# Performance work log

Measured on AMD Instinct MI355X. Metric: run time of the kernel, lower is better.

## Reference

```python
import jax, jax.numpy as jnp
import numpy as np

# Fixed-step Dormand-Prince RK45 (dopri5) over t in [0, 1].
# torchdiffeq's dopri5 is adaptive; an adaptive while-loop is not
# reverse-differentiable in JAX, so we use the same dopri5 tableau with a
# fixed step count, which reproduces the per-step math exactly.
N_STEPS = 64

# dopri5 Butcher tableau (a-matrix rows; b = 5th-order weights = row a7)
A21 = 1/5
A31, A32 = 3/40, 9/40
A41, A42, A43 = 44/45, -56/15, 32/9
A51, A52, A53, A54 = 19372/6561, -25360/2187, 64448/6561, -212/729
A61, A62, A63, A64, A65 = 9017/3168, -355/33, 46732/5247, 49/176, -5103/18656
B1, B3, B4, B5, B6 = 35/384, 500/1113, 125/192, -2187/6784, 11/84


def setup_inputs() -> dict:
    key = jax.random.key(0)
    ks = jax.random.split(key, 7)
    data_dim, hidden_dim, batch = 512, 1024, 4096
    s1 = 1.0 / np.sqrt(data_dim)
    s2 = 1.0 / np.sqrt(hidden_dim)
    return {
        "x":  jax.random.normal(ks[0], (batch, data_dim), jnp.float32),
        "W1": jax.random.normal(ks[1], (hidden_dim, data_dim), jnp.float32) * s1,
        "b1": jax.random.normal(ks[2], (hidden_dim,), jnp.float32) * s1,
        "W2": jax.random.normal(ks[3], (hidden_dim, hidden_dim), jnp.float32) * s2,
        "b2": jax.random.normal(ks[4], (hidden_dim,), jnp.float32) * s2,
        "W3": jax.random.normal(ks[5], (data_dim, hidden_dim), jnp.float32) * s2,
        "b3": jax.random.normal(ks[6], (data_dim,), jnp.float32) * s2,
    }


def reference(x, W1, b1, W2, b2, W3, b3):
    def f(y):  # ODEFunc MLP: fc1 -> relu -> fc2 -> relu -> fc3 (autonomous)
        h = jax.nn.relu(y @ W1.T + b1)
        h = jax.nn.relu(h @ W2.T + b2)
        return h @ W3.T + b3

    h = jnp.float32(1.0 / N_STEPS)

    def step(y, _):
        k1 = f(y)
        k2 = f(y + h * (A21 * k1))
        k3 = f(y + h * (A31 * k1 + A32 * k2))
        k4 = f(y + h * (A41 * k1 + A42 * k2 + A43 * k3))
        k5 = f(y + h * (A51 * k1 + A52 * k2 + A53 * k3 + A54 * k4))
        k6 = f(y + h * (A61 * k1 + A62 * k2 + A63 * k3 + A64 * k4 + A65 * k5))
        y_next = y + h * (B1 * k1 + B3 * k3 + B4 * k4 + B5 * k5 + B6 * k6)
        return y_next, None

    y_final, _ = jax.lax.scan(step, x, None, length=N_STEPS)
    return y_final
```

## Files before the change

### kernel.cpp

```cpp
#include <hip/hip_runtime.h>
#include <hip/hip_bf16.h>
#include <stdint.h>
#include <stddef.h>

using bf16_t = __hip_bfloat16;
typedef __attribute__((ext_vector_type(8))) short short8;
typedef __attribute__((ext_vector_type(4))) float f32x4;

__device__ __forceinline__ void gload_lds16(void* lds, const void* g) {
  __builtin_amdgcn_global_load_lds(
      (const __attribute__((address_space(1))) unsigned int*)g,
      (__attribute__((address_space(3))) unsigned int*)lds,
      16, 0, 0);
}

template<bool RELU, bool COMBINE, bool STORE_K, bool STORE_YF>
__global__ __launch_bounds__(256, 4)
void gemm_bt(const bf16_t* __restrict__ A, const bf16_t* __restrict__ B,
             const float* __restrict__ bias,
             bf16_t* __restrict__ obf,
             bf16_t* __restrict__ kout,
             float* __restrict__ yf_out,
             const float* __restrict__ y_in,
             const bf16_t* __restrict__ kp0, const bf16_t* __restrict__ kp1,
             const bf16_t* __restrict__ kp2, const bf16_t* __restrict__ kp3,
             float c0, float c1, float c2, float c3, float ccur,
             int M, int N, int K, int lgx)
{
  __shared__ __align__(16) bf16_t As[2][64 * 64];
  __shared__ __align__(16) bf16_t Bs[2][64 * 64];

  const int t    = threadIdx.x;
  const int lane = t & 63;
  const int wid  = t >> 6;
  const int wm   = wid >> 1;
  const int wn   = wid & 1;

  const int nwg = gridDim.x, bid = blockIdx.x;
  const int swz = (bid & 7) * (nwg >> 3) + (bid >> 3);
  const int gxm = (1 << lgx) - 1;
  const int bx  = swz & gxm;
  const int by  = swz >> lgx;
  const int bn0 = bx * 64, bm0 = by * 64;

  const bf16_t* Ag = A + (size_t)bm0 * K;
  const bf16_t* Bg = B + (size_t)bn0 * K;

  f32x4 acc[2][2] = {};

  auto stage = [&](int b, int kt) {
    const int k0 = kt * 64;
#pragma unroll
    for (int r = 0; r < 2; ++r) {
      int ch  = t + r * 256;
      int row = ch >> 3, s = ch & 7;
      int sl  = s ^ (row & 7);
      gload_lds16(&As[b][ch * 8], Ag + (size_t)row * K + k0 + sl * 8);
    }
#pragma unroll
    for (int r = 0; r < 2; ++r) {
      int ch  = t + r * 256;
      int row = ch >> 3, s = ch & 7;
      int sl  = s ^ (row & 7);
      gload_lds16(&Bs[b][ch * 8], Bg + (size_t)row * K + k0 + sl * 8);
    }
  };

  const int nt = K >> 6;
  stage(0, 0);

  const int ro = lane & 15;
  const int ks = lane >> 4;

  for (int tt = 0; tt < nt; ++tt) {
    const int c = tt & 1;
    asm volatile("s_waitcnt vmcnt(0)" ::: "memory");
    __builtin_amdgcn_s_barrier();
    asm volatile("" ::: "memory");

    if (tt + 1 < nt) stage(c ^ 1, tt + 1);

#pragma unroll
    for (int kk = 0; kk < 2; ++kk) {
      short8 af[2], bfr[2];
      const int slot = kk * 4 + ks;
#pragma unroll
      for (int mi = 0; mi < 2; ++mi) {
        int row = wm * 32 + mi * 16 + ro;
        int ch  = row * 8 + (slot ^ (row & 7));
        af[mi]  = *(const short8*)&As[c][ch * 8];
      }
#pragma unroll
      for (int ni = 0; ni < 2; ++ni) {
        int row = wn * 32 + ni * 16 + ro;
        int ch  = row * 8 + (slot ^ (row & 7));
        bfr[ni] = *(const short8*)&Bs[c][ch * 8];
      }
      __builtin_amdgcn_s_setprio(1);
#pragma unroll
      for (int mi = 0; mi < 2; ++mi)
#pragma unroll
        for (int ni = 0; ni < 2; ++ni)
          acc[mi][ni] = __builtin_amdgcn_mfma_f32_16x16x32_bf16(
              af[mi], bfr[ni], acc[mi][ni], 0, 0, 0);
      __builtin_amdgcn_s_setprio(0);
    }
  }

  const int rb = bm0 + wm * 32;
  const int cb = bn0 + wn * 32;
#pragma unroll
  for (int mi = 0; mi < 2; ++mi) {
#pragma unroll
    for (int ni = 0; ni < 2; ++ni) {
      const int col = cb + ni * 16 + ro;
      const float bv = bias[col];
#pragma unroll
      for (int r = 0; r < 4; ++r) {
        const int row = rb + mi * 16 + (lane >> 4) * 4 + r;
        const size_t idx = (size_t)row * N + col;
        float v = acc[mi][ni][r] + bv;
        if (RELU) v = fmaxf(v, 0.f);
        if (COMBINE) {
          if (STORE_K) kout[idx] = __float2bfloat16(v);
          float z = y_in[idx] + ccur * v;
          if (kp0) z += c0 * __bfloat162float(kp0[idx]);
          if (kp1) z += c1 * __bfloat162float(kp1[idx]);
          if (kp2) z += c2 * __bfloat162float(kp2[idx]);
          if (kp3) z += c3 * __bfloat162float(kp3[idx]);
          if (STORE_YF) yf_out[idx] = z;
          obf[idx] = __float2bfloat16(z);
        } else {
          obf[idx] = __float2bfloat16(v);
        }
      }
    }
  }
}

__global__ void init_y_kernel(const float* __restrict__ x, float* __restrict__ y,
                              bf16_t* __restrict__ yb, int n) {
  int i = blockIdx.x * blockDim.x + threadIdx.x;
  if (i < n) {
    float v = x[i];
    y[i]  = v;
    yb[i] = __float2bfloat16(v);
  }
}

__global__ void f2b_kernel(const float* __restrict__ in, bf16_t* __restrict__ out, int n) {
  int i = blockIdx.x * blockDim.x + threadIdx.x;
  if (i < n) out[i] = __float2bfloat16(in[i]);
}

extern "C" void kernel_launch(void* const* d_in, const int* in_sizes, int n_in,
                              void* d_out, int out_size, void* d_ws, size_t ws_size,
                              hipStream_t stream)
{
  const float* x  = (const float*)d_in[0];
  const float* W1 = (const float*)d_in[1];
  const float* b1 = (const float*)d_in[2];
  const float* W2 = (const float*)d_in[3];
  const float* b2 = (const float*)d_in[4];
  const float* W3 = (const float*)d_in[5];
  const float* b3 = (const float*)d_in[6];

  const int data   = in_sizes[6];
  const int hidden = in_sizes[2];
  const int batch  = in_sizes[0] / data;

  char* ws = (char*)d_ws;
  size_t off = 0;
  auto alloc = [&](size_t bytes) -> void* {
    off = (off + 255) & ~(size_t)255;
    void* p = ws + off;
    off += bytes;
    return p;
  };
  const size_t nyd = (size_t)batch * data;
  const size_t nh  = (size_t)batch * hidden;

  float*  y   = (float*)alloc(nyd * 4);
  bf16_t* yb  = (bf16_t*)alloc(nyd * 2);
  bf16_t* zb  = (bf16_t*)alloc(nyd * 2);
  bf16_t* h1  = (bf16_t*)alloc(nh * 2);
  bf16_t* h2  = (bf16_t*)alloc(nh * 2);
  bf16_t* k1  = (bf16_t*)alloc(nyd * 2);
  bf16_t* k2  = (bf16_t*)alloc(nyd * 2);
  bf16_t* k3  = (bf16_t*)alloc(nyd * 2);
  bf16_t* k4  = (bf16_t*)alloc(nyd * 2);
  bf16_t* k5  = (bf16_t*)alloc(nyd * 2);
  bf16_t* W1b = (bf16_t*)alloc((size_t)hidden * data * 2);
  bf16_t* W2b = (bf16_t*)alloc((size_t)hidden * hidden * 2);
  bf16_t* W3b = (bf16_t*)alloc((size_t)data * hidden * 2);

  {
    int n = (int)nyd;
    init_y_kernel<<<(n + 255) / 256, 256, 0, stream>>>(x, y, yb, n);
    n = hidden * data;
    f2b_kernel<<<(n + 255) / 256, 256, 0, stream>>>(W1, W1b, n);
    n = hidden * hidden;
    f2b_kernel<<<(n + 255) / 256, 256, 0, stream>>>(W2, W2b, n);
    n = data * hidden;
    f2b_kernel<<<(n + 255) / 256, 256, 0, stream>>>(W3, W3b, n);
  }

  const double hh = 1.0 / 64.0;
  const float hA21 = (float)(hh * (1.0/5.0));
  const float hA31 = (float)(hh * (3.0/40.0)),    hA32 = (float)(hh * (9.0/40.0));
  const float hA41 = (float)(hh * (44.0/45.0)),   hA42 = (float)(hh * (-56.0/15.0)),
              hA43 = (float)(hh * (32.0/9.0));
  const float hA51 = (float)(hh * (19372.0/6561.0)),  hA52 = (float)(hh * (-25360.0/2187.0)),
              hA53 = (float)(hh * (64448.0/6561.0)),  hA54 = (float)(hh * (-212.0/729.0));
  const float hA61 = (float)(hh * (9017.0/3168.0)),   hA62 = (float)(hh * (-355.0/33.0)),
              hA63 = (float)(hh * (46732.0/5247.0)),  hA64 = (float)(hh * (49.0/176.0)),
              hA65 = (float)(hh * (-5103.0/18656.0));
  const float hB1 = (float)(hh * (35.0/384.0)),   hB3 = (float)(hh * (500.0/1113.0)),
              hB4 = (float)(hh * (125.0/192.0)),  hB5 = (float)(hh * (-2187.0/6784.0)),
              hB6 = (float)(hh * (11.0/84.0));

  const dim3 blk(256);
  const int gridH = (hidden / 64) * (batch / 64);
  const int grid3 = (data / 64) * (batch / 64);
  const int lgxH = 4, lgx3 = 3;

  auto mlp_front = [&](const bf16_t* zin) {
    gemm_bt<true, false, false, false><<<gridH, blk, 0, stream>>>(
        zin, W1b, b1, h1, nullptr, nullptr, nullptr,
        nullptr, nullptr, nullptr, nullptr, 0.f, 0.f, 0.f, 0.f, 0.f,
        batch, hidden, data, lgxH);
    gemm_bt<true, false, false, false><<<gridH, blk, 0, stream>>>(
        h1, W2b, b2, h2, nullptr, nullptr, nullptr,
        nullptr, nullptr, nullptr, nullptr, 0.f, 0.f, 0.f, 0.f, 0.f,
        batch, hidden, hidden, lgxH);
  };

  auto stage_k = [&](bf16_t* kout, const bf16_t* p0, float cc0, const bf16_t* p1, float cc1,
                     const bf16_t* p2, float cc2, const bf16_t* p3, float cc3, float ccur) {
    gemm_bt<false, true, true, false><<<grid3, blk, 0, stream>>>(
        h2, W3b, b3, zb, kout, nullptr, y,
        p0, p1, p2, p3, cc0, cc1, cc2, cc3, ccur,
        batch, data, hidden, lgx3);
  };

  for (int step = 0; step < 64; ++step) {
    mlp_front(yb);
    stage_k(k1, nullptr, 0.f, nullptr, 0.f, nullptr, 0.f, nullptr, 0.f, hA21);
    mlp_front(zb);
    stage_k(k2, k1, hA31, nullptr, 0.f, nullptr, 0.f, nullptr, 0.f, hA32);
    mlp_front(zb);
    stage_k(k3, k1, hA41, k2, hA42, nullptr, 0.f, nullptr, 0.f, hA43);
    mlp_front(zb);
    stage_k(k4, k1, hA51, k2, hA52, k3, hA53, nullptr, 0.f, hA54);
    mlp_front(zb);
    stage_k(k5, k1, hA61, k2, hA62, k3, hA63, k4, hA64, hA65);
    mlp_front(zb);
    float* yf = (step == 63) ? (float*)d_out : y;
    gemm_bt<false, true, false, true><<<grid3, blk, 0, stream>>>(
        h2, W3b, b3, yb, nullptr, yf, y,
        k1, k3, k4, k5, hB1, hB3, hB4, hB5, hB6,
        batch, data, hidden, lgx3);
  }
}
```

Before: 18.26 ms.

## Fuse all RK stages into one persistent megakernel with per-group barriers

Result: slower. 54.34 ms (+197.5%).

```diff
diff --git a/kernel.cpp b/kernel.cpp
--- a/kernel.cpp
+++ b/kernel.cpp
@@ -14,71 +14,72 @@
       16, 0, 0);
 }
 
-template<bool RELU, bool COMBINE, bool STORE_K, bool STORE_YF>
-__global__ __launch_bounds__(256, 4)
-void gemm_bt(const bf16_t* __restrict__ A, const bf16_t* __restrict__ B,
-             const float* __restrict__ bias,
-             bf16_t* __restrict__ obf,
-             bf16_t* __restrict__ kout,
-             float* __restrict__ yf_out,
-             const float* __restrict__ y_in,
-             const bf16_t* __restrict__ kp0, const bf16_t* __restrict__ kp1,
-             const bf16_t* __restrict__ kp2, const bf16_t* __restrict__ kp3,
-             float c0, float c1, float c2, float c3, float ccur,
-             int M, int N, int K, int lgx)
+constexpr int BATCH = 4096, DATA = 512, HID = 1024;
+constexpr int NBLK  = 512;
+constexpr int BPG   = 64;
+constexpr int GROWS = 512;
+
+struct MegaArgs {
+  const float *x, *W1, *b1, *W2, *b2, *W3, *b3;
+  float* y; bf16_t *yb, *zb, *h1, *h2;
+  bf16_t *k1, *k2, *k3, *k4, *k5;
+  bf16_t *W1b, *W2b, *W3b;
+  float* out;
+  unsigned* bar;
+};
+
+struct Smem { bf16_t As[2][64 * 64]; bf16_t Bs[2][64 * 64]; };
+
+template<bool COMB>
+__device__ __forceinline__ void vgemm(
+    Smem& sm, int j,
+    const bf16_t* __restrict__ A, const bf16_t* __restrict__ B,
+    const float* __restrict__ bias,
+    bf16_t* __restrict__ obf,
+    bf16_t* __restrict__ kdst,
+    const float* __restrict__ yv, float* __restrict__ ywr,
+    float* __restrict__ dout,
+    const bf16_t* kp0, const bf16_t* kp1, const bf16_t* kp2, const bf16_t* kp3,
+    float c0, float c1, float c2, float c3, float ccur,
+    int K, int lgN, int nvt, int N, int lgnt)
 {
-  __shared__ __align__(16) bf16_t As[2][64 * 64];
-  __shared__ __align__(16) bf16_t Bs[2][64 * 64];
-
   const int t    = threadIdx.x;
   const int lane = t & 63;
   const int wid  = t >> 6;
   const int wm   = wid >> 1;
   const int wn   = wid & 1;
-
-  const int nwg = gridDim.x, bid = blockIdx.x;
-  const int swz = (bid & 7) * (nwg >> 3) + (bid >> 3);
-  const int gxm = (1 << lgx) - 1;
-  const int bx  = swz & gxm;
-  const int by  = swz >> lgx;
-  const int bn0 = bx * 64, bm0 = by * 64;
-
-  const bf16_t* Ag = A + (size_t)bm0 * K;
-  const bf16_t* Bg = B + (size_t)bn0 * K;
-
-  f32x4 acc[2][2] = {};
-
-  auto stage = [&](int b, int kt) {
-    const int k0 = kt * 64;
-#pragma unroll
-    for (int r = 0; r < 2; ++r) {
-      int ch  = t + r * 256;
-      int row = ch >> 3, s = ch & 7;
-      int sl  = s ^ (row & 7);
-      gload_lds16(&As[b][ch * 8], Ag + (size_t)row * K + k0 + sl * 8);
-    }
-#pragma unroll
-    for (int r = 0; r < 2; ++r) {
-      int ch  = t + r * 256;
-      int row = ch >> 3, s = ch & 7;
-      int sl  = s ^ (row & 7);
-      gload_lds16(&Bs[b][ch * 8], Bg + (size_t)row * K + k0 + sl * 8);
-    }
-  };
-
-  const int nt = K >> 6;
-  stage(0, 0);
-
+  const int nt    = 1 << lgnt;
+  const int total = nvt << lgnt;
+  const int nmask = (1 << lgN) - 1;
   const int ro = lane & 15;
   const int ks = lane >> 4;
 
-  for (int tt = 0; tt < nt; ++tt) {
-    const int c = tt & 1;
+  auto stage = [&](int b, int gi) {
+    const int vt = j * nvt + (gi >> lgnt);
+    const int kt = gi & (nt - 1);
+    const bf16_t* Ag = A + (size_t)((vt >> lgN) * 64) * K + kt * 64;
+    const bf16_t* Bg = B + (size_t)((vt & nmask) * 64) * K + kt * 64;
+#pragma unroll
+    for (int r = 0; r < 2; ++r) {
+      int ch = t + r * 256, row = ch >> 3, s = ch & 7, sl = s ^ (row & 7);
+      gload_lds16(&sm.As[b][ch * 8], Ag + (size_t)row * K + sl * 8);
+    }
+#pragma unroll
+    for (int r = 0; r < 2; ++r) {
+      int ch = t + r * 256, row = ch >> 3, s = ch & 7, sl = s ^ (row & 7);
+      gload_lds16(&sm.Bs[b][ch * 8], Bg + (size_t)row * K + sl * 8);
+    }
+  };
+
+  f32x4 acc[2][2] = {};
+  stage(0, 0);
+
+  for (int gi = 0; gi < total; ++gi) {
+    const int c = gi & 1;
     asm volatile("s_waitcnt vmcnt(0)" ::: "memory");
     __builtin_amdgcn_s_barrier();
     asm volatile("" ::: "memory");
-
-    if (tt + 1 < nt) stage(c ^ 1, tt + 1);
+    if (gi + 1 < total) stage(c ^ 1, gi + 1);
 
 #pragma unroll
     for (int kk = 0; kk < 2; ++kk) {
@@ -88,13 +89,13 @@
       for (int mi = 0; mi < 2; ++mi) {
         int row = wm * 32 + mi * 16 + ro;
         int ch  = row * 8 + (slot ^ (row & 7));
-        af[mi]  = *(const short8*)&As[c][ch * 8];
+        af[mi]  = *(const short8*)&sm.As[c][ch * 8];
       }
 #pragma unroll
       for (int ni = 0; ni < 2; ++ni) {
         int row = wn * 32 + ni * 16 + ro;
         int ch  = row * 8 + (slot ^ (row & 7));
-        bfr[ni] = *(const short8*)&Bs[c][ch * 8];
+        bfr[ni] = *(const short8*)&sm.Bs[c][ch * 8];
       }
       __builtin_amdgcn_s_setprio(1);
 #pragma unroll
@@ -105,70 +106,159 @@
               af[mi], bfr[ni], acc[mi][ni], 0, 0, 0);
       __builtin_amdgcn_s_setprio(0);
     }
-  }
-
-  const int rb = bm0 + wm * 32;
-  const int cb = bn0 + wn * 32;
-#pragma unroll
-  for (int mi = 0; mi < 2; ++mi) {
-#pragma unroll
-    for (int ni = 0; ni < 2; ++ni) {
-      const int col = cb + ni * 16 + ro;
-      const float bv = bias[col];
-#pragma unroll
-      for (int r = 0; r < 4; ++r) {
-        const int row = rb + mi * 16 + (lane >> 4) * 4 + r;
-        const size_t idx = (size_t)row * N + col;
-        float v = acc[mi][ni][r] + bv;
-        if (RELU) v = fmaxf(v, 0.f);
-        if (COMBINE) {
-          if (STORE_K) kout[idx] = __float2bfloat16(v);
-          float z = y_in[idx] + ccur * v;
-          if (kp0) z += c0 * __bfloat162float(kp0[idx]);
-          if (kp1) z += c1 * __bfloat162float(kp1[idx]);
-          if (kp2) z += c2 * __bfloat162float(kp2[idx]);
-          if (kp3) z += c3 * __bfloat162float(kp3[idx]);
-          if (STORE_YF) yf_out[idx] = z;
-          obf[idx] = __float2bfloat16(z);
-        } else {
-          obf[idx] = __float2bfloat16(v);
+
+    if (((gi + 1) & (nt - 1)) == 0) {
+      const int vt = j * nvt + (gi >> lgnt);
+      const int rb = (vt >> lgN) * 64 + wm * 32;
+      const int cb = (vt & nmask) * 64 + wn * 32;
+#pragma unroll
+      for (int mi = 0; mi < 2; ++mi) {
+#pragma unroll
+        for (int ni = 0; ni < 2; ++ni) {
+          const int col = cb + ni * 16 + ro;
+          const float bv = bias[col];
+#pragma unroll
+          for (int r = 0; r < 4; ++r) {
+            const int row = rb + mi * 16 + (lane >> 4) * 4 + r;
+            const size_t idx = (size_t)row * N + col;
+            float v = acc[mi][ni][r] + bv;
+            if (COMB) {
+              if (kdst) kdst[idx] = __float2bfloat16(v);
+              float z = yv[idx] + ccur * v;
+              if (kp0) z += c0 * __bfloat162float(kp0[idx]);
+              if (kp1) z += c1 * __bfloat162float(kp1[idx]);
+              if (kp2) z += c2 * __bfloat162float(kp2[idx]);
+              if (kp3) z += c3 * __bfloat162float(kp3[idx]);
+              if (ywr)  ywr[idx]  = z;
+              if (dout) dout[idx] = z;
+              obf[idx] = __float2bfloat16(z);
+            } else {
+              obf[idx] = __float2bfloat16(fmaxf(v, 0.f));
+            }
+          }
+          acc[mi][ni] = f32x4{0.f, 0.f, 0.f, 0.f};
         }
       }
     }
   }
 }
 
-__global__ void init_y_kernel(const float* __restrict__ x, float* __restrict__ y,
-                              bf16_t* __restrict__ yb, int n) {
-  int i = blockIdx.x * blockDim.x + threadIdx.x;
-  if (i < n) {
-    float v = x[i];
-    y[i]  = v;
-    yb[i] = __float2bfloat16(v);
+__global__ void __launch_bounds__(256, 2) ode_mega(MegaArgs a) {
+  __shared__ Smem sm;
+  const int bid = blockIdx.x;
+  const int g   = bid & 7;
+  const int j   = bid >> 3;
+  unsigned* ctr = a.bar + (size_t)g * 64;
+  unsigned phase = 0;
+
+  auto gbar = [&]() {
+    __syncthreads();
+    ++phase;
+    if (threadIdx.x == 0) {
+      __threadfence();
+      __hip_atomic_fetch_add(ctr, 1u, __ATOMIC_RELAXED, __HIP_MEMORY_SCOPE_AGENT);
+      while (__hip_atomic_load(ctr, __ATOMIC_RELAXED, __HIP_MEMORY_SCOPE_AGENT)
+             < phase * (unsigned)BPG)
+        __builtin_amdgcn_s_sleep(2);
+      __threadfence();
+    }
+    __syncthreads();
+  };
+
+  const size_t god = (size_t)g * GROWS * DATA;
+  const size_t goh = (size_t)g * GROWS * HID;
+
+  {
+    const int gt = j * 256 + (int)threadIdx.x;
+    const int gs = BPG * 256;
+    auto cvt4 = [&](const float* in, bf16_t* outp, int n) {
+      for (int i = gt * 4; i < n; i += gs * 4) {
+        float4 v = *(const float4*)(in + i);
+        bf16_t o[4] = {__float2bfloat16(v.x), __float2bfloat16(v.y),
+                       __float2bfloat16(v.z), __float2bfloat16(v.w)};
+        *(uint64_t*)(outp + i) = *(uint64_t*)o;
+      }
+    };
+    cvt4(a.W1, a.W1b, HID * DATA);
+    cvt4(a.W2, a.W2b, HID * HID);
+    cvt4(a.W3, a.W3b, DATA * HID);
+    const float* xg = a.x + god;
+    float* yg = a.y + god;
+    bf16_t* ybg = a.yb + god;
+    for (int i = gt * 4; i < GROWS * DATA; i += gs * 4) {
+      float4 v = *(const float4*)(xg + i);
+      *(float4*)(yg + i) = v;
+      bf16_t o[4] = {__float2bfloat16(v.x), __float2bfloat16(v.y),
+                     __float2bfloat16(v.z), __float2bfloat16(v.w)};
+      *(uint64_t*)(ybg + i) = *(uint64_t*)o;
+    }
   }
-}
-
-__global__ void f2b_kernel(const float* __restrict__ in, bf16_t* __restrict__ out, int n) {
-  int i = blockIdx.x * blockDim.x + threadIdx.x;
-  if (i < n) out[i] = __float2bfloat16(in[i]);
+  gbar();
+
+  constexpr double hh = 1.0 / 64.0;
+  constexpr float hA21 = (float)(hh * (1.0/5.0));
+  constexpr float hA31 = (float)(hh * (3.0/40.0)),   hA32 = (float)(hh * (9.0/40.0));
+  constexpr float hA41 = (float)(hh * (44.0/45.0)),  hA42 = (float)(hh * (-56.0/15.0)),
+                  hA43 = (float)(hh * (32.0/9.0));
+  constexpr float hA51 = (float)(hh * (19372.0/6561.0)), hA52 = (float)(hh * (-25360.0/2187.0)),
+                  hA53 = (float)(hh * (64448.0/6561.0)), hA54 = (float)(hh * (-212.0/729.0));
+  constexpr float hA61 = (float)(hh * (9017.0/3168.0)),  hA62 = (float)(hh * (-355.0/33.0)),
+                  hA63 = (float)(hh * (46732.0/5247.0)), hA64 = (float)(hh * (49.0/176.0)),
+                  hA65 = (float)(hh * (-5103.0/18656.0));
+  constexpr float hB1 = (float)(hh * (35.0/384.0)),  hB3 = (float)(hh * (500.0/1113.0)),
+                  hB4 = (float)(hh * (125.0/192.0)), hB5 = (float)(hh * (-2187.0/6784.0)),
+                  hB6 = (float)(hh * (11.0/84.0));
+
+  for (int step = 0; step < 64; ++step) {
+    for (int s = 0; s < 6; ++s) {
+      const bf16_t* zin = ((s == 0) ? a.yb : a.zb) + god;
+
+      vgemm<false>(sm, j, zin, a.W1b, a.b1, a.h1 + goh,
+                   nullptr, nullptr, nullptr, nullptr,
+                   nullptr, nullptr, nullptr, nullptr,
+                   0.f, 0.f, 0.f, 0.f, 0.f,
+                   DATA, 4, 2, HID, 3);
+      gbar();
+
+      vgemm<false>(sm, j, a.h1 + goh, a.W2b, a.b2, a.h2 + goh,
+                   nullptr, nullptr, nullptr, nullptr,
+                   nullptr, nullptr, nullptr, nullptr,
+                   0.f, 0.f, 0.f, 0.f, 0.f,
+                   HID, 4, 2, HID, 4);
+      gbar();
+
+      const bf16_t *p0 = nullptr, *p1 = nullptr, *p2 = nullptr, *p3 = nullptr;
+      float c0 = 0.f, c1 = 0.f, c2 = 0.f, c3 = 0.f, ccur;
+      bf16_t* kd = nullptr;
+      switch (s) {
+        case 0: ccur = hA21; kd = a.k1 + god; break;
+        case 1: ccur = hA32; kd = a.k2 + god; p0 = a.k1 + god; c0 = hA31; break;
+        case 2: ccur = hA43; kd = a.k3 + god; p0 = a.k1 + god; c0 = hA41;
+                p1 = a.k2 + god; c1 = hA42; break;
+        case 3: ccur = hA54; kd = a.k4 + god; p0 = a.k1 + god; c0 = hA51;
+                p1 = a.k2 + god; c1 = hA52; p2 = a.k3 + god; c2 = hA53; break;
+        case 4: ccur = hA65; kd = a.k5 + god; p0 = a.k1 + god; c0 = hA61;
+                p1 = a.k2 + god; c1 = hA62; p2 = a.k3 + god; c2 = hA63;
+                p3 = a.k4 + god; c3 = hA64; break;
+        default: ccur = hB6; p0 = a.k1 + god; c0 = hB1; p1 = a.k3 + god; c1 = hB3;
+                 p2 = a.k4 + god; c2 = hB4; p3 = a.k5 + god; c3 = hB5; break;
+      }
+      bf16_t* ob  = ((s == 5) ? a.yb : a.zb) + god;
+      float*  ywr = (s == 5) ? a.y + god : nullptr;
+      float*  dst = (s == 5 && step == 63) ? a.out + god : nullptr;
+      vgemm<true>(sm, j, a.h2 + goh, a.W3b, a.b3, ob,
+                  kd, a.y + god, ywr, dst,
+                  p0, p1, p2, p3, c0, c1, c2, c3, ccur,
+                  HID, 3, 1, DATA, 4);
+      gbar();
+    }
+  }
 }
 
 extern "C" void kernel_launch(void* const* d_in, const int* in_sizes, int n_in,
                               void* d_out, int out_size, void* d_ws, size_t ws_size,
                               hipStream_t stream)
 {
-  const float* x  = (const float*)d_in[0];
-  const float* W1 = (const float*)d_in[1];
-  const float* b1 = (const float*)d_in[2];
-  const float* W2 = (const float*)d_in[3];
-  const float* b2 = (const float*)d_in[4];
-  const float* W3 = (const float*)d_in[5];
-  const float* b3 = (const float*)d_in[6];
-
-  const int data   = in_sizes[6];
-  const int hidden = in_sizes[2];
-  const int batch  = in_sizes[0] / data;
-
   char* ws = (char*)d_ws;
   size_t off = 0;
   auto alloc = [&](size_t bytes) -> void* {
@@ -177,88 +267,34 @@
     off += bytes;
     return p;
   };
-  const size_t nyd = (size_t)batch * data;
-  const size_t nh  = (size_t)batch * hidden;
-
-  float*  y   = (float*)alloc(nyd * 4);
-  bf16_t* yb  = (bf16_t*)alloc(nyd * 2);
-  bf16_t* zb  = (bf16_t*)alloc(nyd * 2);
-  bf16_t* h1  = (bf16_t*)alloc(nh * 2);
-  bf16_t* h2  = (bf16_t*)alloc(nh * 2);
-  bf16_t* k1  = (bf16_t*)alloc(nyd * 2);
-  bf16_t* k2  = (bf16_t*)alloc(nyd * 2);
-  bf16_t* k3  = (bf16_t*)alloc(nyd * 2);
-  bf16_t* k4  = (bf16_t*)alloc(nyd * 2);
-  bf16_t* k5  = (bf16_t*)alloc(nyd * 2);
-  bf16_t* W1b = (bf16_t*)alloc((size_t)hidden * data * 2);
-  bf16_t* W2b = (bf16_t*)alloc((size_t)hidden * hidden * 2);
-  bf16_t* W3b = (bf16_t*)alloc((size_t)data * hidden * 2);
-
-  {
-    int n = (int)nyd;
-    init_y_kernel<<<(n + 255) / 256, 256, 0, stream>>>(x, y, yb, n);
-    n = hidden * data;
-    f2b_kernel<<<(n + 255) / 256, 256, 0, stream>>>(W1, W1b, n);
-    n = hidden * hidden;
-    f2b_kernel<<<(n + 255) / 256, 256, 0, stream>>>(W2, W2b, n);
-    n = data * hidden;
-    f2b_kernel<<<(n + 255) / 256, 256, 0, stream>>>(W3, W3b, n);
-  }
-
-  const double hh = 1.0 / 64.0;
-  const float hA21 = (float)(hh * (1.0/5.0));
-  const float hA31 = (float)(hh * (3.0/40.0)),    hA32 = (float)(hh * (9.0/40.0));
-  const float hA41 = (float)(hh * (44.0/45.0)),   hA42 = (float)(hh * (-56.0/15.0)),
-              hA43 = (float)(hh * (32.0/9.0));
-  const float hA51 = (float)(hh * (19372.0/6561.0)),  hA52 = (float)(hh * (-25360.0/2187.0)),
-              hA53 = (float)(hh * (64448.0/6561.0)),  hA54 = (float)(hh * (-212.0/729.0));
-  const float hA61 = (float)(hh * (9017.0/3168.0)),   hA62 = (float)(hh * (-355.0/33.0)),
-              hA63 = (float)(hh * (46732.0/5247.0)),  hA64 = (float)(hh * (49.0/176.0)),
-              hA65 = (float)(hh * (-5103.0/18656.0));
-  const float hB1 = (float)(hh * (35.0/384.0)),   hB3 = (float)(hh * (500.0/1113.0)),
-              hB4 = (float)(hh * (125.0/192.0)),  hB5 = (float)(hh * (-2187.0/6784.0)),
-              hB6 = (float)(hh * (11.0/84.0));
-
-  const dim3 blk(256);
-  const int gridH = (hidden / 64) * (batch / 64);
-  const int grid3 = (data / 64) * (batch / 64);
-  const int lgxH = 4, lgx3 = 3;
-
-  auto mlp_front = [&](const bf16_t* zin) {
-    gemm_bt<true, false, false, false><<<gridH, blk, 0, stream>>>(
-        zin, W1b, b1, h1, nullptr, nullptr, nullptr,
-        nullptr, nullptr, nullptr, nullptr, 0.f, 0.f, 0.f, 0.f, 0.f,
-        batch, hidden, data, lgxH);
-    gemm_bt<true, false, false, false><<<gridH, blk, 0, stream>>>(
-        h1, W2b, b2, h2, nullptr, nullptr, nullptr,
-        nullptr, nullptr, nullptr, nullptr, 0.f, 0.f, 0.f, 0.f, 0.f,
-        batch, hidden, hidden, lgxH);
-  };
-
-  auto stage_k = [&](bf16_t* kout, const bf16_t* p0, float cc0, const bf16_t* p1, float cc1,
-                     const bf16_t* p2, float cc2, const bf16_t* p3, float cc3, float ccur) {
-    gemm_bt<false, true, true, false><<<grid3, blk, 0, stream>>>(
-        h2, W3b, b3, zb, kout, nullptr, y,
-        p0, p1, p2, p3, cc0, cc1, cc2, cc3, ccur,
-        batch, data, hidden, lgx3);
-  };
-
-  for (int step = 0; step < 64; ++step) {
-    mlp_front(yb);
-    stage_k(k1, nullptr, 0.f, nullptr, 0.f, nullptr, 0.f, nullptr, 0.f, hA21);
-    mlp_front(zb);
-    stage_k(k2, k1, hA31, nullptr, 0.f, nullptr, 0.f, nullptr, 0.f, hA32);
-    mlp_front(zb);
-    stage_k(k3, k1, hA41, k2, hA42, nullptr, 0.f, nullptr, 0.f, hA43);
-    mlp_front(zb);
-    stage_k(k4, k1, hA51, k2, hA52, k3, hA53, nullptr, 0.f, hA54);
-    mlp_front(zb);
-    stage_k(k5, k1, hA61, k2, hA62, k3, hA63, k4, hA64, hA65);
-    mlp_front(zb);
-    float* yf = (step == 63) ? (float*)d_out : y;
-    gemm_bt<false, true, false, true><<<grid3, blk, 0, stream>>>(
-        h2, W3b, b3, yb, nullptr, yf, y,
-        k1, k3, k4, k5, hB1, hB3, hB4, hB5, hB6,
-        batch, data, hidden, lgx3);
-  }
+  const size_t nyd = (size_t)BATCH * DATA;
+  const size_t nh  = (size_t)BATCH * HID;
+
+  MegaArgs a;
+  a.bar = (unsigned*)alloc(4096);
+  a.x  = (const float*)d_in[0];
+  a.W1 = (const float*)d_in[1];
+  a.b1 = (const float*)d_in[2];
+  a.W2 = (const float*)d_in[3];
+  a.b2 = (const float*)d_in[4];
+  a.W3 = (const float*)d_in[5];
+  a.b3 = (const float*)d_in[6];
+
+  a.y   = (float*)alloc(nyd * 4);
+  a.yb  = (bf16_t*)alloc(nyd * 2);
+  a.zb  = (bf16_t*)alloc(nyd * 2);
+  a.h1  = (bf16_t*)alloc(nh * 2);
+  a.h2  = (bf16_t*)alloc(nh * 2);
+  a.k1  = (bf16_t*)alloc(nyd * 2);
+  a.k2  = (bf16_t*)alloc(nyd * 2);
+  a.k3  = (bf16_t*)alloc(nyd * 2);
+  a.k4  = (bf16_t*)alloc(nyd * 2);
+  a.k5  = (bf16_t*)alloc(nyd * 2);
+  a.W1b = (bf16_t*)alloc((size_t)HID * DATA * 2);
+  a.W2b = (bf16_t*)alloc((size_t)HID * HID * 2);
+  a.W3b = (bf16_t*)alloc((size_t)DATA * HID * 2);
+  a.out = (float*)d_out;
+
+  hipMemsetAsync(a.bar, 0, 4096, stream);
+  ode_mega<<<dim3(NBLK), dim3(256), 0, stream>>>(a);
 }
```
